# Kernel tuning notes

Hardware: AMD Instinct MI355X
Metric: run time of the kernel (lower is better)

The kernel has to match this reference:

```python
import jax, jax.numpy as jnp
import numpy as np

H = 128
B, N = 8, 200
EPS = 1e-5


def _linear(v, W, b):
    return v @ W.T + b


def _masked_bn(v, m, gamma, beta):
    # v: (..., H); m: (...,) float 0/1 mask. BatchNorm1d over masked rows only
    # (track_running_stats=False -> batch statistics, biased variance).
    mf = m[..., None]
    axes = tuple(range(v.ndim - 1))
    cnt = jnp.maximum(jnp.sum(m), 1.0)
    mean = jnp.sum(v * mf, axis=axes) / cnt            # (H,)
    var = jnp.sum(mf * (v - mean) ** 2, axis=axes) / cnt
    vn = (v - mean) * jax.lax.rsqrt(var + EPS) * gamma + beta
    return jnp.where(mf > 0, vn, v)


def setup_inputs() -> dict:
    key = jax.random.key(0)
    ks = jax.random.split(key, 16)
    s = 1.0 / np.sqrt(H)
    p = lambda k, shp: jax.random.uniform(k, shp, jnp.float32, -s, s)
    return {
        "x": jax.random.normal(ks[0], (B, N, H), jnp.float32),
        "e": jax.random.normal(ks[1], (B, N, N, H), jnp.float32),
        "mask": jax.random.randint(ks[2], (B, N), 0, 2, jnp.int32),
        "Ue_W": p(ks[3], (H, H)), "Ue_b": p(ks[4], (H,)),
        "Ve_W": p(ks[5], (H, H)), "Ve_b": p(ks[6], (H,)),
        "Un_W": p(ks[7], (H, H)), "Un_b": p(ks[8], (H,)),
        "Vn_W": p(ks[9], (H, H)), "Vn_b": p(ks[10], (H,)),
        "bn_n_g": jnp.ones((H,), jnp.float32), "bn_n_b": jnp.zeros((H,), jnp.float32),
        "bn_e_g": jnp.ones((H,), jnp.float32), "bn_e_b": jnp.zeros((H,), jnp.float32),
    }


def reference(x, e, mask, Ue_W, Ue_b, Ve_W, Ve_b, Un_W, Un_b, Vn_W, Vn_b,
              bn_n_g, bn_n_b, bn_e_g, bn_e_b):
    m = mask.astype(x.dtype)                      # (B,N)
    m1 = m[..., None]                             # (B,N,1)
    sq_mask = m[:, :, None] * m[:, None, :]       # (B,N,N)

    # EdgeFeatures: e_ij = U*e_ij + V*x_i + V*x_j (with node-masked Vx)
    Vx = m1 * _linear(x, Ve_W, Ve_b)              # (B,N,H)
    e_tmp = _linear(e, Ue_W, Ue_b) + Vx[:, :, None, :] + Vx[:, None, :, :]

    gate = jax.nn.sigmoid(e_tmp)                  # (B,N,N,H)
    gate_m = gate * sq_mask[..., None]            # mask rows and cols

    # NodeFeatures, sum aggregation: x_i = U*x_i + sum_j gate_ij * (V*x_j)
    Ux = m1 * _linear(x, Un_W, Un_b)
    Vxn = m1 * _linear(x, Vn_W, Vn_b)
    agg = jnp.einsum("bijh,bjh->bih", gate_m, Vxn)
    x_tmp = Ux + agg

    e_bn = _masked_bn(e_tmp, sq_mask, bn_e_g, bn_e_b)
    x_bn = _masked_bn(x_tmp, m, bn_n_g, bn_n_b)

    x_new = x + jax.nn.relu(x_bn)
    e_new = e + jax.nn.relu(e_bn)
    return x_new, e_new
```

## Files before the change

kernel.cpp:

```cpp
#include <hip/hip_runtime.h>
#include <hip/hip_bf16.h>

namespace {

typedef __attribute__((ext_vector_type(8))) short short8;
typedef __attribute__((ext_vector_type(4))) float f32x4;

constexpr int H = 128;
constexpr int N = 200;
constexpr int BN = 1600;
constexpr int X_SIZE = BN * H;
constexpr int NH = N * H;

constexpr int WS_VX    = 0;
constexpr int WS_UX    = WS_VX + X_SIZE;
constexpr int WS_VXN   = WS_UX + X_SIZE;
constexpr int WS_XTMP  = WS_VXN + X_SIZE;
constexpr int WS_ESUMS = WS_XTMP + X_SIZE;
constexpr int WS_ESSQS = WS_ESUMS + 32 * H;
constexpr int WS_NSUMS = WS_ESSQS + 32 * H;
constexpr int WS_NSSQS = WS_NSUMS + 32 * H;
constexpr int WS_STAT_END = WS_NSSQS + 32 * H;
constexpr int WS_ESC   = WS_STAT_END;
constexpr int WS_ESH   = WS_ESC + H;
constexpr int WS_NSC   = WS_ESH + H;
constexpr int WS_NSH   = WS_NSC + H;

__device__ __forceinline__ unsigned short f2bf(float f) {
  __hip_bfloat16 h = __float2bfloat16(f);
  return __builtin_bit_cast(unsigned short, h);
}

__device__ __forceinline__ short8 pack8(f32x4 a, f32x4 b) {
  short8 r;
  r[0] = (short)f2bf(a[0]); r[1] = (short)f2bf(a[1]);
  r[2] = (short)f2bf(a[2]); r[3] = (short)f2bf(a[3]);
  r[4] = (short)f2bf(b[0]); r[5] = (short)f2bf(b[1]);
  r[6] = (short)f2bf(b[2]); r[7] = (short)f2bf(b[3]);
  return r;
}

__global__ __launch_bounds__(128) void k_prep(
    const float* __restrict__ x, const int* __restrict__ mask,
    const float* __restrict__ VeW, const float* __restrict__ Veb,
    const float* __restrict__ UnW, const float* __restrict__ Unb,
    const float* __restrict__ VnW, const float* __restrict__ Vnb,
    float* __restrict__ ws) {
  const int bi = blockIdx.x, h = threadIdx.x;
  __shared__ float xr[H];
  xr[h] = x[bi * H + h];
  __syncthreads();
  const float mi = (float)mask[bi];
  float a0 = 0.f, a1 = 0.f, a2 = 0.f;
  #pragma unroll 4
  for (int k = 0; k < H; k += 4) {
    const float x0 = xr[k], x1 = xr[k + 1], x2 = xr[k + 2], x3 = xr[k + 3];
    float4 w;
    w = *(const float4*)&VeW[h * H + k];
    a0 += w.x * x0 + w.y * x1 + w.z * x2 + w.w * x3;
    w = *(const float4*)&UnW[h * H + k];
    a1 += w.x * x0 + w.y * x1 + w.z * x2 + w.w * x3;
    w = *(const float4*)&VnW[h * H + k];
    a2 += w.x * x0 + w.y * x1 + w.z * x2 + w.w * x3;
  }
  ws[WS_VX  + bi * H + h] = mi * (a0 + Veb[h]);
  ws[WS_UX  + bi * H + h] = mi * (a1 + Unb[h]);
  ws[WS_VXN + bi * H + h] = mi * (a2 + Vnb[h]);
}

__global__ __launch_bounds__(256, 3) void k_edge0(
    const float* __restrict__ e, const int* __restrict__ mask,
    const float* __restrict__ UeW, const float* __restrict__ Ueb,
    float* __restrict__ ws) {
  const int bi = blockIdx.x;
  const int b = bi / N;
  const int tid = threadIdx.x;
  const int w = tid >> 6, lane = tid & 63;
  const int l15 = lane & 15, lg = lane >> 4;
  const int hbase = w * 32;

  __shared__ float etile[2][2048];
  __shared__ float mrow[N];
  __shared__ float sS[H], sS2[H], sA[H];

  const float mi = (float)mask[bi];
  const float* __restrict__ eg = e + (size_t)bi * NH;

  auto stage = [&](int buf, int jt) {
    const int j0 = jt * 16;
    #pragma unroll
    for (int ii = 0; ii < 2; ++ii) {
      const int instr = 2 * w + ii;
      const int row = 2 * instr + (lane >> 5);
      const int c16 = lane & 31;
      const int gr = min(j0 + row, N - 1);
      const int sc16 = c16 ^ (row & 7);
      const float* src = eg + (size_t)gr * H + sc16 * 4;
      float* dst = &etile[buf][instr * 256];
      __builtin_amdgcn_global_load_lds(
          (const __attribute__((address_space(1))) void*)src,
          (__attribute__((address_space(3))) void*)dst, 16, 0, 0);
    }
  };

  stage(0, 0);
  if (tid < N) mrow[tid] = (float)mask[b * N + tid];

  short8 Wf[2][4];
  #pragma unroll
  for (int ht = 0; ht < 2; ++ht) {
    const float* wr = &UeW[(size_t)(hbase + ht * 16 + l15) * H + lg * 8];
    #pragma unroll
    for (int s = 0; s < 4; ++s) {
      const f32x4 u0 = *(const f32x4*)(wr + s * 32);
      const f32x4 u1 = *(const f32x4*)(wr + s * 32 + 4);
      Wf[ht][s] = pack8(u0, u1);
    }
  }
  f32x4 base4[2];
  #pragma unroll
  for (int ht = 0; ht < 2; ++ht) {
    const int h0 = hbase + ht * 16 + 4 * lg;
    const f32x4 ub = *(const f32x4*)&Ueb[h0];
    const f32x4 vx = *(const f32x4*)&ws[WS_VX + (size_t)bi * H + h0];
    base4[ht] = ub + vx;
  }

  float bnS[2][4] = {{0,0,0,0},{0,0,0,0}};
  float bnS2[2][4] = {{0,0,0,0},{0,0,0,0}};
  float ag[2][4] = {{0,0,0,0},{0,0,0,0}};

  __syncthreads();

  for (int jt = 0; jt < 13; ++jt) {
    const int cur = jt & 1;
    if (jt + 1 < 13) stage(cur ^ 1, jt + 1);

    const float* tp = &etile[cur][0];
    short8 Ef[4];
    #pragma unroll
    for (int s = 0; s < 4; ++s) {
      const int c0 = (lg * 2 + s * 8) ^ (l15 & 7);
      const int c1 = (lg * 2 + s * 8 + 1) ^ (l15 & 7);
      const f32x4 u0 = *(const f32x4*)&tp[l15 * 128 + c0 * 4];
      const f32x4 u1 = *(const f32x4*)&tp[l15 * 128 + c1 * 4];
      Ef[s] = pack8(u0, u1);
    }

    f32x4 acc[2] = {f32x4(0.f), f32x4(0.f)};
    #pragma unroll
    for (int s = 0; s < 4; ++s) {
      #pragma unroll
      for (int ht = 0; ht < 2; ++ht)
        acc[ht] = __builtin_amdgcn_mfma_f32_16x16x32_bf16(Wf[ht][s], Ef[s], acc[ht], 0, 0, 0);
    }

    const int j = jt * 16 + l15;
    const bool valid = (j < N);
    const int jc = valid ? j : N - 1;
    const float msk = valid ? mi * mrow[jc] : 0.f;
    const float* rv = &ws[WS_VX + (size_t)(b * N + jc) * H];
    const float* rn = &ws[WS_VXN + (size_t)(b * N + jc) * H];
    #pragma unroll
    for (int ht = 0; ht < 2; ++ht) {
      const int h0 = hbase + ht * 16 + 4 * lg;
      const f32x4 vx4 = *(const f32x4*)&rv[h0];
      const f32x4 vn4 = *(const f32x4*)&rn[h0];
      #pragma unroll
      for (int r = 0; r < 4; ++r) {
        const float v = acc[ht][r] + base4[ht][r] + vx4[r];
        bnS[ht][r]  += msk * v;
        bnS2[ht][r] += msk * v * v;
        const float sg = __builtin_amdgcn_rcpf(1.f + __expf(-v));
        ag[ht][r] += msk * sg * vn4[r];
      }
    }
    __syncthreads();
  }

  #pragma unroll
  for (int ht = 0; ht < 2; ++ht) {
    #pragma unroll
    for (int r = 0; r < 4; ++r) {
      #pragma unroll
      for (int mm = 1; mm <= 8; mm <<= 1) {
        bnS[ht][r]  += __shfl_xor(bnS[ht][r], mm);
        bnS2[ht][r] += __shfl_xor(bnS2[ht][r], mm);
        ag[ht][r]   += __shfl_xor(ag[ht][r], mm);
      }
    }
  }
  if (l15 == 0) {
    #pragma unroll
    for (int ht = 0; ht < 2; ++ht) {
      #pragma unroll
      for (int r = 0; r < 4; ++r) {
        const int h = hbase + ht * 16 + 4 * lg + r;
        sS[h] = bnS[ht][r]; sS2[h] = bnS2[ht][r]; sA[h] = ag[ht][r];
      }
    }
  }
  __syncthreads();
  if (tid < H) {
    const int slot = (bi & 31) * H + tid;
    atomicAdd(&ws[WS_ESUMS + slot], sS[tid]);
    atomicAdd(&ws[WS_ESSQS + slot], sS2[tid]);
    const float v = ws[WS_UX + (size_t)bi * H + tid] + sA[tid];
    ws[WS_XTMP + (size_t)bi * H + tid] = v;
    atomicAdd(&ws[WS_NSUMS + slot], mi * v);
    atomicAdd(&ws[WS_NSSQS + slot], mi * v * v);
  }
}

__global__ void k_stats(const int* __restrict__ mask,
                        const float* __restrict__ beg, const float* __restrict__ beb,
                        const float* __restrict__ bng, const float* __restrict__ bnb,
                        float* __restrict__ ws) {
  __shared__ float sb[8];
  const int t = threadIdx.x;
  const int b = t >> 5, li = t & 31;
  float s = 0.f;
  for (int i = li; i < N; i += 32) s += (float)mask[b * N + i];
  #pragma unroll
  for (int o = 16; o >= 1; o >>= 1) s += __shfl_down(s, o, 32);
  if (li == 0) sb[b] = s;
  __syncthreads();
  if (t < H) {
    float cn = 0.f, ce = 0.f;
    #pragma unroll
    for (int bb = 0; bb < 8; ++bb) { cn += sb[bb]; ce += sb[bb] * sb[bb]; }
    ce = fmaxf(ce, 1.f); cn = fmaxf(cn, 1.f);
    float es = 0.f, es2 = 0.f, ns = 0.f, ns2 = 0.f;
    #pragma unroll 4
    for (int k = 0; k < 32; ++k) {
      es  += ws[WS_ESUMS + k * H + t];
      es2 += ws[WS_ESSQS + k * H + t];
      ns  += ws[WS_NSUMS + k * H + t];
      ns2 += ws[WS_NSSQS + k * H + t];
    }
    const float me = es / ce;
    const float ve = fmaxf(es2 / ce - me * me, 0.f);
    const float se = rsqrtf(ve + 1e-5f) * beg[t];
    ws[WS_ESC + t] = se;
    ws[WS_ESH + t] = beb[t] - me * se;
    const float mn = ns / cn;
    const float vn = fmaxf(ns2 / cn - mn * mn, 0.f);
    const float sn = rsqrtf(vn + 1e-5f) * bng[t];
    ws[WS_NSC + t] = sn;
    ws[WS_NSH + t] = bnb[t] - mn * sn;
  }
}

__global__ void k_x2(const float* __restrict__ x, const int* __restrict__ mask,
                     const float* __restrict__ ws, float* __restrict__ out) {
  const int idx = blockIdx.x * 256 + threadIdx.x;
  if (idx >= X_SIZE) return;
  const int h = idx & 127, bi = idx >> 7;
  const float v = ws[WS_XTMP + idx];
  const float r = (mask[bi] != 0) ? (v * ws[WS_NSC + h] + ws[WS_NSH + h]) : v;
  out[idx] = x[idx] + fmaxf(r, 0.f);
}

__global__ __launch_bounds__(256, 3) void k_edge1(
    const float* __restrict__ e, const int* __restrict__ mask,
    const float* __restrict__ UeW, const float* __restrict__ Ueb,
    const float* __restrict__ ws, float* __restrict__ out) {
  const int bi = blockIdx.x;
  const int b = bi / N;
  const int tid = threadIdx.x;
  const int w = tid >> 6, lane = tid & 63;
  const int l15 = lane & 15, lg = lane >> 4;
  const int hbase = w * 32;

  __shared__ float etile[2][2048];
  __shared__ float mrow[N];

  const float mi = (float)mask[bi];
  const float* __restrict__ eg = e + (size_t)bi * NH;

  auto stage = [&](int buf, int jt) {
    const int j0 = jt * 16;
    #pragma unroll
    for (int ii = 0; ii < 2; ++ii) {
      const int instr = 2 * w + ii;
      const int row = 2 * instr + (lane >> 5);
      const int c16 = lane & 31;
      const int gr = min(j0 + row, N - 1);
      const int sc16 = c16 ^ (row & 7);
      const float* src = eg + (size_t)gr * H + sc16 * 4;
      float* dst = &etile[buf][instr * 256];
      __builtin_amdgcn_global_load_lds(
          (const __attribute__((address_space(1))) void*)src,
          (__attribute__((address_space(3))) void*)dst, 16, 0, 0);
    }
  };

  stage(0, 0);
  if (tid < N) mrow[tid] = (float)mask[b * N + tid];

  short8 Wf[2][4];
  #pragma unroll
  for (int ht = 0; ht < 2; ++ht) {
    const float* wr = &UeW[(size_t)(hbase + ht * 16 + l15) * H + lg * 8];
    #pragma unroll
    for (int s = 0; s < 4; ++s) {
      const f32x4 u0 = *(const f32x4*)(wr + s * 32);
      const f32x4 u1 = *(const f32x4*)(wr + s * 32 + 4);
      Wf[ht][s] = pack8(u0, u1);
    }
  }
  f32x4 base4[2], sc4[2], sh4[2];
  #pragma unroll
  for (int ht = 0; ht < 2; ++ht) {
    const int h0 = hbase + ht * 16 + 4 * lg;
    const f32x4 ub = *(const f32x4*)&Ueb[h0];
    const f32x4 vx = *(const f32x4*)&ws[WS_VX + (size_t)bi * H + h0];
    base4[ht] = ub + vx;
    sc4[ht] = *(const f32x4*)&ws[WS_ESC + h0];
    sh4[ht] = *(const f32x4*)&ws[WS_ESH + h0];
  }

  __syncthreads();

  for (int jt = 0; jt < 13; ++jt) {
    const int cur = jt & 1;
    if (jt + 1 < 13) stage(cur ^ 1, jt + 1);

    const float* tp = &etile[cur][0];
    short8 Ef[4];
    #pragma unroll
    for (int s = 0; s < 4; ++s) {
      const int c0 = (lg * 2 + s * 8) ^ (l15 & 7);
      const int c1 = (lg * 2 + s * 8 + 1) ^ (l15 & 7);
      const f32x4 u0 = *(const f32x4*)&tp[l15 * 128 + c0 * 4];
      const f32x4 u1 = *(const f32x4*)&tp[l15 * 128 + c1 * 4];
      Ef[s] = pack8(u0, u1);
    }

    f32x4 acc[2] = {f32x4(0.f), f32x4(0.f)};
    #pragma unroll
    for (int s = 0; s < 4; ++s) {
      #pragma unroll
      for (int ht = 0; ht < 2; ++ht)
        acc[ht] = __builtin_amdgcn_mfma_f32_16x16x32_bf16(Wf[ht][s], Ef[s], acc[ht], 0, 0, 0);
    }

    const int j = jt * 16 + l15;
    if (j < N) {
      const float msk = mi * mrow[j];
      const float* rv = &ws[WS_VX + (size_t)(b * N + j) * H];
      float* __restrict__ og = out + (size_t)X_SIZE + (size_t)bi * NH + (size_t)j * H;
      #pragma unroll
      for (int ht = 0; ht < 2; ++ht) {
        const int h0 = hbase + ht * 16 + 4 * lg;
        const f32x4 vx4 = *(const f32x4*)&rv[h0];
        const int ch = (h0 >> 2) ^ (l15 & 7);
        const f32x4 e4 = *(const f32x4*)&tp[l15 * 128 + ch * 4];
        f32x4 o;
        #pragma unroll
        for (int r = 0; r < 4; ++r) {
          const float v = acc[ht][r] + base4[ht][r] + vx4[r];
          const float rr = (msk > 0.f) ? (v * sc4[ht][r] + sh4[ht][r]) : v;
          o[r] = e4[r] + fmaxf(rr, 0.f);
        }
        *(f32x4*)&og[h0] = o;
      }
    }
    __syncthreads();
  }
}

}

extern "C" void kernel_launch(void* const* d_in, const int* in_sizes, int n_in,
                              void* d_out, int out_size, void* d_ws, size_t ws_size,
                              hipStream_t stream) {
  const float* x    = (const float*)d_in[0];
  const float* e    = (const float*)d_in[1];
  const int*   mask = (const int*)d_in[2];
  const float* UeW  = (const float*)d_in[3];
  const float* Ueb  = (const float*)d_in[4];
  const float* VeW  = (const float*)d_in[5];
  const float* Veb  = (const float*)d_in[6];
  const float* UnW  = (const float*)d_in[7];
  const float* Unb  = (const float*)d_in[8];
  const float* VnW  = (const float*)d_in[9];
  const float* Vnb  = (const float*)d_in[10];
  const float* bng  = (const float*)d_in[11];
  const float* bnb  = (const float*)d_in[12];
  const float* beg  = (const float*)d_in[13];
  const float* beb  = (const float*)d_in[14];
  float* ws  = (float*)d_ws;
  float* out = (float*)d_out;

  hipMemsetAsync(ws + WS_ESUMS, 0, (WS_STAT_END - WS_ESUMS) * sizeof(float), stream);
  k_prep<<<BN, 128, 0, stream>>>(x, mask, VeW, Veb, UnW, Unb, VnW, Vnb, ws);
  k_edge0<<<BN, 256, 0, stream>>>(e, mask, UeW, Ueb, ws);
  k_stats<<<1, 256, 0, stream>>>(mask, beg, beb, bng, bnb, ws);
  k_x2<<<800, 256, 0, stream>>>(x, mask, ws, out);
  k_edge1<<<BN, 256, 0, stream>>>(e, mask, UeW, Ueb, ws, out);
}
```

Baseline: 205.4 us.

## Merge edge passes into templated kernel with 8 waves and direct global loads

Replaces the two edge kernels with one templated kernel launched at 512 threads. Each block's 8 waves are split into 4 column quarters times 2 interleaved j-tile halves. The LDS double-buffered async staging and the per-tile __syncthreads are removed; each lane now loads its e rows straight from global memory into registers. In pass 0 the partial stats from the two j-halves are combined through shared memory. This aims for more parallelism and less synchronisation, at the cost of losing the prefetch overlap and possibly less coalesced global reads (the pass-1 residual e is re-read from global).

```diff
diff --git a/kernel.cpp b/kernel.cpp
--- a/kernel.cpp
+++ b/kernel.cpp
@@ -11,6 +11,7 @@
 constexpr int BN = 1600;
 constexpr int X_SIZE = BN * H;
 constexpr int NH = N * H;
+constexpr int NT = 13;
 
 constexpr int WS_VX    = 0;
 constexpr int WS_UX    = WS_VX + X_SIZE;
@@ -68,43 +69,26 @@
   ws[WS_VXN + bi * H + h] = mi * (a2 + Vnb[h]);
 }
 
-__global__ __launch_bounds__(256, 3) void k_edge0(
+template <int PASS>
+__global__ __launch_bounds__(512) void k_edge(
     const float* __restrict__ e, const int* __restrict__ mask,
     const float* __restrict__ UeW, const float* __restrict__ Ueb,
-    float* __restrict__ ws) {
+    float* __restrict__ ws, float* __restrict__ out) {
   const int bi = blockIdx.x;
   const int b = bi / N;
   const int tid = threadIdx.x;
   const int w = tid >> 6, lane = tid & 63;
   const int l15 = lane & 15, lg = lane >> 4;
-  const int hbase = w * 32;
-
-  __shared__ float etile[2][2048];
+  const int hq = w & 3, jhalf = w >> 2;
+  const int hbase = hq * 32;
+
   __shared__ float mrow[N];
-  __shared__ float sS[H], sS2[H], sA[H];
+  __shared__ float pS[8][32], pS2[8][32], pA[8][32];
+
+  if (tid < N) mrow[tid] = (float)mask[b * N + tid];
 
   const float mi = (float)mask[bi];
   const float* __restrict__ eg = e + (size_t)bi * NH;
-
-  auto stage = [&](int buf, int jt) {
-    const int j0 = jt * 16;
-    #pragma unroll
-    for (int ii = 0; ii < 2; ++ii) {
-      const int instr = 2 * w + ii;
-      const int row = 2 * instr + (lane >> 5);
-      const int c16 = lane & 31;
-      const int gr = min(j0 + row, N - 1);
-      const int sc16 = c16 ^ (row & 7);
-      const float* src = eg + (size_t)gr * H + sc16 * 4;
-      float* dst = &etile[buf][instr * 256];
-      __builtin_amdgcn_global_load_lds(
-          (const __attribute__((address_space(1))) void*)src,
-          (__attribute__((address_space(3))) void*)dst, 16, 0, 0);
-    }
-  };
-
-  stage(0, 0);
-  if (tid < N) mrow[tid] = (float)mask[b * N + tid];
 
   short8 Wf[2][4];
   #pragma unroll
@@ -117,13 +101,17 @@
       Wf[ht][s] = pack8(u0, u1);
     }
   }
-  f32x4 base4[2];
+  f32x4 base4[2], sc4[2], sh4[2];
   #pragma unroll
   for (int ht = 0; ht < 2; ++ht) {
     const int h0 = hbase + ht * 16 + 4 * lg;
     const f32x4 ub = *(const f32x4*)&Ueb[h0];
     const f32x4 vx = *(const f32x4*)&ws[WS_VX + (size_t)bi * H + h0];
     base4[ht] = ub + vx;
+    if (PASS == 1) {
+      sc4[ht] = *(const f32x4*)&ws[WS_ESC + h0];
+      sh4[ht] = *(const f32x4*)&ws[WS_ESH + h0];
+    }
   }
 
   float bnS[2][4] = {{0,0,0,0},{0,0,0,0}};
@@ -132,20 +120,20 @@
 
   __syncthreads();
 
-  for (int jt = 0; jt < 13; ++jt) {
-    const int cur = jt & 1;
-    if (jt + 1 < 13) stage(cur ^ 1, jt + 1);
-
-    const float* tp = &etile[cur][0];
+  for (int jt = jhalf; jt < NT; jt += 2) {
+    const int j = jt * 16 + l15;
+    const int jc = min(j, N - 1);
+
+    const float* er = eg + (size_t)jc * H + lg * 8;
+    f32x4 raw[8];
+    #pragma unroll
+    for (int s = 0; s < 4; ++s) {
+      raw[2 * s]     = *(const f32x4*)(er + s * 32);
+      raw[2 * s + 1] = *(const f32x4*)(er + s * 32 + 4);
+    }
     short8 Ef[4];
     #pragma unroll
-    for (int s = 0; s < 4; ++s) {
-      const int c0 = (lg * 2 + s * 8) ^ (l15 & 7);
-      const int c1 = (lg * 2 + s * 8 + 1) ^ (l15 & 7);
-      const f32x4 u0 = *(const f32x4*)&tp[l15 * 128 + c0 * 4];
-      const f32x4 u1 = *(const f32x4*)&tp[l15 * 128 + c1 * 4];
-      Ef[s] = pack8(u0, u1);
-    }
+    for (int s = 0; s < 4; ++s) Ef[s] = pack8(raw[2 * s], raw[2 * s + 1]);
 
     f32x4 acc[2] = {f32x4(0.f), f32x4(0.f)};
     #pragma unroll
@@ -155,60 +143,84 @@
         acc[ht] = __builtin_amdgcn_mfma_f32_16x16x32_bf16(Wf[ht][s], Ef[s], acc[ht], 0, 0, 0);
     }
 
-    const int j = jt * 16 + l15;
-    const bool valid = (j < N);
-    const int jc = valid ? j : N - 1;
-    const float msk = valid ? mi * mrow[jc] : 0.f;
-    const float* rv = &ws[WS_VX + (size_t)(b * N + jc) * H];
-    const float* rn = &ws[WS_VXN + (size_t)(b * N + jc) * H];
-    #pragma unroll
-    for (int ht = 0; ht < 2; ++ht) {
-      const int h0 = hbase + ht * 16 + 4 * lg;
-      const f32x4 vx4 = *(const f32x4*)&rv[h0];
-      const f32x4 vn4 = *(const f32x4*)&rn[h0];
+    if (PASS == 0) {
+      const float msk = (j < N) ? mi * mrow[jc] : 0.f;
+      const float* rv = &ws[WS_VX + (size_t)(b * N + jc) * H];
+      const float* rn = &ws[WS_VXN + (size_t)(b * N + jc) * H];
       #pragma unroll
-      for (int r = 0; r < 4; ++r) {
-        const float v = acc[ht][r] + base4[ht][r] + vx4[r];
-        bnS[ht][r]  += msk * v;
-        bnS2[ht][r] += msk * v * v;
-        const float sg = __builtin_amdgcn_rcpf(1.f + __expf(-v));
-        ag[ht][r] += msk * sg * vn4[r];
+      for (int ht = 0; ht < 2; ++ht) {
+        const int h0 = hbase + ht * 16 + 4 * lg;
+        const f32x4 vx4 = *(const f32x4*)&rv[h0];
+        const f32x4 vn4 = *(const f32x4*)&rn[h0];
+        #pragma unroll
+        for (int r = 0; r < 4; ++r) {
+          const float v = acc[ht][r] + base4[ht][r] + vx4[r];
+          bnS[ht][r]  += msk * v;
+          bnS2[ht][r] += msk * v * v;
+          const float sg = __builtin_amdgcn_rcpf(1.f + __expf(-v));
+          ag[ht][r] += msk * sg * vn4[r];
+        }
       }
-    }
-    __syncthreads();
-  }
-
-  #pragma unroll
-  for (int ht = 0; ht < 2; ++ht) {
-    #pragma unroll
-    for (int r = 0; r < 4; ++r) {
-      #pragma unroll
-      for (int mm = 1; mm <= 8; mm <<= 1) {
-        bnS[ht][r]  += __shfl_xor(bnS[ht][r], mm);
-        bnS2[ht][r] += __shfl_xor(bnS2[ht][r], mm);
-        ag[ht][r]   += __shfl_xor(ag[ht][r], mm);
+    } else {
+      if (j < N) {
+        const float msk = mi * mrow[j];
+        const float* rv = &ws[WS_VX + (size_t)(b * N + j) * H];
+        float* __restrict__ og = out + (size_t)X_SIZE + (size_t)bi * NH + (size_t)j * H;
+        #pragma unroll
+        for (int ht = 0; ht < 2; ++ht) {
+          const int h0 = hbase + ht * 16 + 4 * lg;
+          const f32x4 vx4 = *(const f32x4*)&rv[h0];
+          const f32x4 e4  = *(const f32x4*)&eg[(size_t)j * H + h0];
+          f32x4 o;
+          #pragma unroll
+          for (int r = 0; r < 4; ++r) {
+            const float v = acc[ht][r] + base4[ht][r] + vx4[r];
+            const float rr = (msk > 0.f) ? (v * sc4[ht][r] + sh4[ht][r]) : v;
+            o[r] = e4[r] + fmaxf(rr, 0.f);
+          }
+          *(f32x4*)&og[h0] = o;
+        }
       }
     }
   }
-  if (l15 == 0) {
+
+  if (PASS == 0) {
     #pragma unroll
     for (int ht = 0; ht < 2; ++ht) {
       #pragma unroll
       for (int r = 0; r < 4; ++r) {
-        const int h = hbase + ht * 16 + 4 * lg + r;
-        sS[h] = bnS[ht][r]; sS2[h] = bnS2[ht][r]; sA[h] = ag[ht][r];
+        #pragma unroll
+        for (int mm = 1; mm <= 8; mm <<= 1) {
+          bnS[ht][r]  += __shfl_xor(bnS[ht][r], mm);
+          bnS2[ht][r] += __shfl_xor(bnS2[ht][r], mm);
+          ag[ht][r]   += __shfl_xor(ag[ht][r], mm);
+        }
       }
     }
-  }
-  __syncthreads();
-  if (tid < H) {
-    const int slot = (bi & 31) * H + tid;
-    atomicAdd(&ws[WS_ESUMS + slot], sS[tid]);
-    atomicAdd(&ws[WS_ESSQS + slot], sS2[tid]);
-    const float v = ws[WS_UX + (size_t)bi * H + tid] + sA[tid];
-    ws[WS_XTMP + (size_t)bi * H + tid] = v;
-    atomicAdd(&ws[WS_NSUMS + slot], mi * v);
-    atomicAdd(&ws[WS_NSSQS + slot], mi * v * v);
+    if (l15 == 0) {
+      #pragma unroll
+      for (int ht = 0; ht < 2; ++ht) {
+        #pragma unroll
+        for (int r = 0; r < 4; ++r) {
+          const int idx = ht * 16 + 4 * lg + r;
+          pS[w][idx] = bnS[ht][r]; pS2[w][idx] = bnS2[ht][r]; pA[w][idx] = ag[ht][r];
+        }
+      }
+    }
+    __syncthreads();
+    if (tid < H) {
+      const int hq2 = tid >> 5, idx = tid & 31;
+      const float s1 = pS[hq2][idx] + pS[hq2 + 4][idx];
+      const float s2 = pS2[hq2][idx] + pS2[hq2 + 4][idx];
+      const float s3 = pA[hq2][idx] + pA[hq2 + 4][idx];
+      const int slot = (bi & 31) * H + tid;
+      atomicAdd(&ws[WS_ESUMS + slot], s1);
+      atomicAdd(&ws[WS_ESSQS + slot], s2);
+      const float v = ws[WS_UX + (size_t)bi * H + tid] + s3;
+      ws[WS_XTMP + (size_t)bi * H + tid] = v;
+      atomicAdd(&ws[WS_NSUMS + slot], mi * v);
+      atomicAdd(&ws[WS_NSSQS + slot], mi * v * v);
+    }
   }
 }
 
@@ -259,115 +271,6 @@
   const float v = ws[WS_XTMP + idx];
   const float r = (mask[bi] != 0) ? (v * ws[WS_NSC + h] + ws[WS_NSH + h]) : v;
   out[idx] = x[idx] + fmaxf(r, 0.f);
-}
-
-__global__ __launch_bounds__(256, 3) void k_edge1(
-    const float* __restrict__ e, const int* __restrict__ mask,
-    const float* __restrict__ UeW, const float* __restrict__ Ueb,
-    const float* __restrict__ ws, float* __restrict__ out) {
-  const int bi = blockIdx.x;
-  const int b = bi / N;
-  const int tid = threadIdx.x;
-  const int w = tid >> 6, lane = tid & 63;
-  const int l15 = lane & 15, lg = lane >> 4;
-  const int hbase = w * 32;
-
-  __shared__ float etile[2][2048];
-  __shared__ float mrow[N];
-
-  const float mi = (float)mask[bi];
-  const float* __restrict__ eg = e + (size_t)bi * NH;
-
-  auto stage = [&](int buf, int jt) {
-    const int j0 = jt * 16;
-    #pragma unroll
-    for (int ii = 0; ii < 2; ++ii) {
-      const int instr = 2 * w + ii;
-      const int row = 2 * instr + (lane >> 5);
-      const int c16 = lane & 31;
-      const int gr = min(j0 + row, N - 1);
-      const int sc16 = c16 ^ (row & 7);
-      const float* src = eg + (size_t)gr * H + sc16 * 4;
-      float* dst = &etile[buf][instr * 256];
-      __builtin_amdgcn_global_load_lds(
-          (const __attribute__((address_space(1))) void*)src,
-          (__attribute__((address_space(3))) void*)dst, 16, 0, 0);
-    }
-  };
-
-  stage(0, 0);
-  if (tid < N) mrow[tid] = (float)mask[b * N + tid];
-
-  short8 Wf[2][4];
-  #pragma unroll
-  for (int ht = 0; ht < 2; ++ht) {
-    const float* wr = &UeW[(size_t)(hbase + ht * 16 + l15) * H + lg * 8];
-    #pragma unroll
-    for (int s = 0; s < 4; ++s) {
-      const f32x4 u0 = *(const f32x4*)(wr + s * 32);
-      const f32x4 u1 = *(const f32x4*)(wr + s * 32 + 4);
-      Wf[ht][s] = pack8(u0, u1);
-    }
-  }
-  f32x4 base4[2], sc4[2], sh4[2];
-  #pragma unroll
-  for (int ht = 0; ht < 2; ++ht) {
-    const int h0 = hbase + ht * 16 + 4 * lg;
-    const f32x4 ub = *(const f32x4*)&Ueb[h0];
-    const f32x4 vx = *(const f32x4*)&ws[WS_VX + (size_t)bi * H + h0];
-    base4[ht] = ub + vx;
-    sc4[ht] = *(const f32x4*)&ws[WS_ESC + h0];
-    sh4[ht] = *(const f32x4*)&ws[WS_ESH + h0];
-  }
-
-  __syncthreads();
-
-  for (int jt = 0; jt < 13; ++jt) {
-    const int cur = jt & 1;
-    if (jt + 1 < 13) stage(cur ^ 1, jt + 1);
-
-    const float* tp = &etile[cur][0];
-    short8 Ef[4];
-    #pragma unroll
-    for (int s = 0; s < 4; ++s) {
-      const int c0 = (lg * 2 + s * 8) ^ (l15 & 7);
-      const int c1 = (lg * 2 + s * 8 + 1) ^ (l15 & 7);
-      const f32x4 u0 = *(const f32x4*)&tp[l15 * 128 + c0 * 4];
-      const f32x4 u1 = *(const f32x4*)&tp[l15 * 128 + c1 * 4];
-      Ef[s] = pack8(u0, u1);
-    }
-
-    f32x4 acc[2] = {f32x4(0.f), f32x4(0.f)};
-    #pragma unroll
-    for (int s = 0; s < 4; ++s) {
-      #pragma unroll
-      for (int ht = 0; ht < 2; ++ht)
-        acc[ht] = __builtin_amdgcn_mfma_f32_16x16x32_bf16(Wf[ht][s], Ef[s], acc[ht], 0, 0, 0);
-    }
-
-    const int j = jt * 16 + l15;
-    if (j < N) {
-      const float msk = mi * mrow[j];
-      const float* rv = &ws[WS_VX + (size_t)(b * N + j) * H];
-      float* __restrict__ og = out + (size_t)X_SIZE + (size_t)bi * NH + (size_t)j * H;
-      #pragma unroll
-      for (int ht = 0; ht < 2; ++ht) {
-        const int h0 = hbase + ht * 16 + 4 * lg;
-        const f32x4 vx4 = *(const f32x4*)&rv[h0];
-        const int ch = (h0 >> 2) ^ (l15 & 7);
-        const f32x4 e4 = *(const f32x4*)&tp[l15 * 128 + ch * 4];
-        f32x4 o;
-        #pragma unroll
-        for (int r = 0; r < 4; ++r) {
-          const float v = acc[ht][r] + base4[ht][r] + vx4[r];
-          const float rr = (msk > 0.f) ? (v * sc4[ht][r] + sh4[ht][r]) : v;
-          o[r] = e4[r] + fmaxf(rr, 0.f);
-        }
-        *(f32x4*)&og[h0] = o;
-      }
-    }
-    __syncthreads();
-  }
 }
 
 }
@@ -395,8 +298,8 @@
 
   hipMemsetAsync(ws + WS_ESUMS, 0, (WS_STAT_END - WS_ESUMS) * sizeof(float), stream);
   k_prep<<<BN, 128, 0, stream>>>(x, mask, VeW, Veb, UnW, Unb, VnW, Vnb, ws);
-  k_edge0<<<BN, 256, 0, stream>>>(e, mask, UeW, Ueb, ws);
+  k_edge<0><<<BN, 512, 0, stream>>>(e, mask, UeW, Ueb, ws, out);
   k_stats<<<1, 256, 0, stream>>>(mask, beg, beb, bng, bnb, ws);
   k_x2<<<800, 256, 0, stream>>>(x, mask, ws, out);
-  k_edge1<<<BN, 256, 0, stream>>>(e, mask, UeW, Ueb, ws, out);
-}
+  k_edge<1><<<BN, 512, 0, stream>>>(e, mask, UeW, Ueb, ws, out);
+}
```

After: 363.1 us. 76.8% more time.
